# Kernel optimization log

Hardware: AMD Instinct MI355X
Metric: run time of the kernel (lower is better)

## Reference

```python
import jax, jax.numpy as jnp
import numpy as np
import math
from functools import partial

SIGMA0 = 12.0
KSIZE = int(2 * (4.0 * SIGMA0 + 0.5))  # 97, already odd
if KSIZE % 2 == 0:
    KSIZE -= 1


def _gauss1d(ksize, sigma):
    # kornia-style gaussian; ksize is odd so no half-pixel shift
    x = jnp.arange(ksize, dtype=jnp.float32) - ksize // 2
    g = jnp.exp(-(x ** 2) / (2.0 * sigma ** 2))
    return g / g.sum()


def _blur(x, sigma):
    # x: (N,1,H,W). filter2d with outer(kx,ky) kernel and constant(zero) border
    # == two separable 1D convs with zero 'SAME' padding.
    k = _gauss1d(KSIZE, sigma)
    dn = ('NCHW', 'OIHW', 'NCHW')
    x = jax.lax.conv_general_dilated(x, k[None, None, :, None], (1, 1), 'SAME', dimension_numbers=dn)
    x = jax.lax.conv_general_dilated(x, k[None, None, None, :], (1, 1), 'SAME', dimension_numbers=dn)
    return x


def _grid_sample_bilinear(img, grid):
    # img: (N,C,H,W); grid: (N,H,W,2) with last dim (x,y) in [-1,1], align_corners=True
    N, C, H, W = img.shape
    x = (grid[..., 0] + 1.0) * 0.5 * (W - 1)
    y = (grid[..., 1] + 1.0) * 0.5 * (H - 1)
    x0 = jnp.floor(x); y0 = jnp.floor(y)
    wx = x - x0; wy = y - y0
    x0i = jnp.clip(x0, 0, W - 1).astype(jnp.int32)
    x1i = jnp.clip(x0 + 1, 0, W - 1).astype(jnp.int32)
    y0i = jnp.clip(y0, 0, H - 1).astype(jnp.int32)
    y1i = jnp.clip(y0 + 1, 0, H - 1).astype(jnp.int32)
    flat = img.reshape(N, C, H * W)

    def gather(yi, xi):
        idx = (yi * W + xi).reshape(N, 1, H * W)
        return jnp.take_along_axis(flat, idx, axis=2).reshape(N, C, H, W)

    wx = wx[:, None]; wy = wy[:, None]  # broadcast over C
    top = gather(y0i, x0i) * (1 - wx) + gather(y0i, x1i) * wx
    bot = gather(y1i, x0i) * (1 - wx) + gather(y1i, x1i) * wx
    return top * (1 - wy) + bot * wy


def _elastic(t, d_rand, sigma, alpha):
    # t: (1,C,H,W); d_rand: (1,2,H,W) uniform [0,1]
    n, c, h, w = t.shape
    d = d_rand * 2.0 - 1.0
    dy = _blur(d[:, 0:1], sigma[0]) * alpha[0]   # (1,1,H,W)
    dx = _blur(d[:, 1:2], sigma[1]) * alpha[1]
    d_yx = jnp.concatenate([dy, dx], axis=1).transpose(0, 2, 3, 1)  # (1,H,W,2) = (dy,dx)
    xs = jnp.linspace(-1.0, 1.0, w, dtype=t.dtype)
    ys = jnp.linspace(-1.0, 1.0, h, dtype=t.dtype)
    gx, gy = jnp.meshgrid(xs, ys)  # (H,W)
    grid = jnp.stack([gx, gy], axis=-1)[None]  # (1,H,W,2) (x,y)
    # NOTE: faithful to source: dy is added to x-coord, dx to y-coord
    return _grid_sample_bilinear(t, jnp.clip(grid + d_yx, -1.0, 1.0))


def setup_inputs() -> dict:
    key = jax.random.key(0)
    k1, k2, k3 = jax.random.split(key, 3)
    H = W = 2048
    return {
        'image': jax.random.normal(k1, (3, H, W), dtype=jnp.float32),
        'mask': (jax.random.uniform(k2, (1, H, W)) > 0.5).astype(jnp.float32),
        'd_rand': jax.random.uniform(k3, (1, 2, H, W), dtype=jnp.float32),
        'log_sigma': jnp.full((2,), math.log(12.0), dtype=jnp.float32),
        'log_alpha': jnp.zeros((2,), dtype=jnp.float32),
    }


def reference(image, mask, d_rand, log_sigma, log_alpha):
    sigma = jnp.exp(log_sigma)
    alpha = jnp.exp(log_alpha)
    img_out = _elastic(image[None], d_rand, sigma, alpha)[0]
    msk_out = _elastic(mask[None], d_rand, sigma, alpha)[0]
    return (img_out, msk_out)
```

## Files before the change

### kernel.cpp

```cpp
#include <hip/hip_runtime.h>

#define H 2048
#define W 2048
#define KS 97
#define KH 48
#define KPAD 112
#define TR 16
#define NB_VB 1024
#define NB_PK 4096

__global__ __launch_bounds__(128) void make_weights_k(const float* __restrict__ log_sigma,
                                                      const float* __restrict__ log_alpha,
                                                      float* __restrict__ wts) {
    __shared__ float e0s[KS], e1s[KS];
    __shared__ float sums[2];
    const int t = threadIdx.x;
    const float s0 = expf(log_sigma[0]);
    const float s1 = expf(log_sigma[1]);
    if (t < KS) {
        const float xx = (float)(t - KH);
        e0s[t] = expf(-(xx * xx) / (2.f * s0 * s0));
        e1s[t] = expf(-(xx * xx) / (2.f * s1 * s1));
    }
    __syncthreads();
    if (t == 0) {
        float a = 0.f, b = 0.f;
        for (int k = 0; k < KS; ++k) { a += e0s[k]; b += e1s[k]; }
        sums[0] = a; sums[1] = b;
    }
    __syncthreads();
    if (t < KPAD) {
        wts[t]        = (t < KS) ? e0s[t] / sums[0] : 0.f;
        wts[KPAD + t] = (t < KS) ? e1s[t] / sums[1] : 0.f;
    }
    if (t == 0) {
        wts[2 * KPAD]     = expf(log_alpha[0]);
        wts[2 * KPAD + 1] = expf(log_alpha[1]);
    }
}

template <bool GUARD>
__device__ __forceinline__ float2 vload_row(const float* __restrict__ src, int row, int col) {
    float2 v = make_float2(0.f, 0.f);
    if (!GUARD || ((unsigned)row < (unsigned)H)) {
        const float2 r2 = *(const float2*)(src + (size_t)row * W + col);
        v.x = fmaf(r2.x, 2.f, -1.f);
        v.y = fmaf(r2.y, 2.f, -1.f);
    }
    return v;
}

template <bool GUARD>
__device__ __forceinline__ void vblur_body(const float* __restrict__ src,
                                           const float* __restrict__ g,
                                           float* __restrict__ dst,
                                           int col, int i0) {
    const int base = i0 - KH;
    float2 win[16];
    float2 acc[TR];
#pragma unroll
    for (int t = 0; t < TR; ++t) acc[t] = make_float2(0.f, 0.f);
#pragma unroll
    for (int t = 0; t < 15; ++t) win[t] = vload_row<GUARD>(src, base + t, col);

    for (int m = 0; m < KPAD / 16; ++m) {
        const int kb = m * 16;
#pragma unroll
        for (int r = 0; r < 16; ++r) {
            const int k = kb + r;
            win[(r + 15) & 15] = vload_row<GUARD>(src, base + k + 15, col);
            const float gk = g[k];
#pragma unroll
            for (int t = 0; t < TR; ++t) {
                const float2 u = win[(r + t) & 15];
                acc[t].x = fmaf(gk, u.x, acc[t].x);
                acc[t].y = fmaf(gk, u.y, acc[t].y);
            }
        }
    }
#pragma unroll
    for (int t = 0; t < TR; ++t)
        *(float2*)(dst + (size_t)(i0 + t) * W + col) = acc[t];
}

__global__ __launch_bounds__(256, 4) void pv_k(const float* __restrict__ drand,
                                               const float* __restrict__ wts,
                                               const float* __restrict__ image,
                                               const float* __restrict__ mask,
                                               float* __restrict__ tmp,
                                               float4* __restrict__ packed) {
    const size_t HW = (size_t)H * W;
    const int bid = blockIdx.x;
    if (bid < NB_VB) {
        const int c   = bid >> 9;
        const int id  = bid & 511;
        const int xcd = id & 7;
        const int seq = id >> 3;
        const int yb  = xcd * 16 + (seq >> 2);
        const int xb  = seq & 3;
        const int col = (xb * 256 + threadIdx.x) * 2;
        const int i0  = yb * TR;
        const float* __restrict__ src = drand + (size_t)c * HW;
        const float* __restrict__ g   = wts + c * KPAD;
        float* __restrict__ dst       = tmp + (size_t)c * HW;
        if (i0 >= KH && i0 + 78 <= H - 1)
            vblur_body<false>(src, g, dst, col, i0);
        else
            vblur_body<true>(src, g, dst, col, i0);
    } else {
        const size_t idx4 = ((size_t)(bid - NB_VB) * 256 + threadIdx.x) * 4;
        const float4 p0 = *(const float4*)(image + idx4);
        const float4 p1 = *(const float4*)(image + HW + idx4);
        const float4 p2 = *(const float4*)(image + 2 * HW + idx4);
        const float4 pm = *(const float4*)(mask + idx4);
        packed[idx4 + 0] = make_float4(p0.x, p1.x, p2.x, pm.x);
        packed[idx4 + 1] = make_float4(p0.y, p1.y, p2.y, pm.y);
        packed[idx4 + 2] = make_float4(p0.z, p1.z, p2.z, pm.z);
        packed[idx4 + 3] = make_float4(p0.w, p1.w, p2.w, pm.w);
    }
}

#define SW 2160
template <bool PACKED>
__global__ __launch_bounds__(512) void hblur_sample_k(const float* __restrict__ tmp,
                                                      const float* __restrict__ wts,
                                                      const float* __restrict__ image,
                                                      const float* __restrict__ mask,
                                                      const float4* __restrict__ packed,
                                                      float* __restrict__ out) {
    const int i   = (blockIdx.x & 7) * 256 + (blockIdx.x >> 3);
    const int tid = threadIdx.x;

    __shared__ __align__(16) float s0[SW];
    __shared__ __align__(16) float s1[SW];
    __shared__ __align__(16) float g0s[KPAD];
    __shared__ __align__(16) float g1s[KPAD];

    if (tid < KPAD) { g0s[tid] = wts[tid]; g1s[tid] = wts[KPAD + tid]; }

    const float* __restrict__ t0 = tmp + (size_t)i * W;
    const float* __restrict__ t1 = tmp + (size_t)H * W + (size_t)i * W;
    for (int idx = tid; idx < SW / 4; idx += 512) {
        const int colb = idx * 4 - KH;
        float4 v0 = make_float4(0.f, 0.f, 0.f, 0.f);
        float4 v1 = v0;
        if (colb >= 0 && colb + 3 < W) {
            v0 = *(const float4*)(t0 + colb);
            v1 = *(const float4*)(t1 + colb);
        }
        *(float4*)(s0 + idx * 4) = v0;
        *(float4*)(s1 + idx * 4) = v1;
    }
    __syncthreads();

    const int lb = tid * 4;

    float4 A0 = *(const float4*)(s0 + lb), B0 = *(const float4*)(s0 + lb + 4);
    float4 A1 = *(const float4*)(s1 + lb), B1 = *(const float4*)(s1 + lb + 4);
    float dy[4] = {0.f, 0.f, 0.f, 0.f}, dx[4] = {0.f, 0.f, 0.f, 0.f};

#pragma unroll
    for (int kg = 0; kg < 26; ++kg) {
        const int k0 = kg * 4;
        const float4 g0q = *(const float4*)(g0s + k0);
        const float4 g1q = *(const float4*)(g1s + k0);
        const float4 N0  = *(const float4*)(s0 + lb + k0 + 8);
        const float4 N1  = *(const float4*)(s1 + lb + k0 + 8);
        const float e0[8] = {A0.x, A0.y, A0.z, A0.w, B0.x, B0.y, B0.z, B0.w};
        const float e1[8] = {A1.x, A1.y, A1.z, A1.w, B1.x, B1.y, B1.z, B1.w};
#pragma unroll
        for (int j = 0; j < 4; ++j) {
            const float gj0 = j == 0 ? g0q.x : j == 1 ? g0q.y : j == 2 ? g0q.z : g0q.w;
            const float gj1 = j == 0 ? g1q.x : j == 1 ? g1q.y : j == 2 ? g1q.z : g1q.w;
#pragma unroll
            for (int c = 0; c < 4; ++c) {
                dy[c] = fmaf(gj0, e0[c + j], dy[c]);
                dx[c] = fmaf(gj1, e1[c + j], dx[c]);
            }
        }
        A0 = B0; B0 = N0; A1 = B1; B1 = N1;
    }

    const float a0 = wts[2 * KPAD];
    const float a1 = wts[2 * KPAD + 1];
    const float step = 2.f / 2047.f;
    float res[4][4];
#pragma unroll
    for (int c = 0; c < 4; ++c) {
        const int j = lb + c;
        const float dyc = dy[c] * a0;
        const float dxc = dx[c] * a1;
        float xn = -1.f + (float)j * step + dyc;
        float yn = -1.f + (float)i * step + dxc;
        xn = fminf(fmaxf(xn, -1.f), 1.f);
        yn = fminf(fmaxf(yn, -1.f), 1.f);

        const float x = (xn + 1.f) * 0.5f * (float)(W - 1);
        const float y = (yn + 1.f) * 0.5f * (float)(H - 1);
        const float x0f = floorf(x), y0f = floorf(y);
        const float wx = x - x0f, wy = y - y0f;

        int x0 = (int)x0f, y0 = (int)y0f;
        int x1 = x0 + 1, y1 = y0 + 1;
        x0 = min(max(x0, 0), W - 1); x1 = min(max(x1, 0), W - 1);
        y0 = min(max(y0, 0), H - 1); y1 = min(max(y1, 0), H - 1);

        const float w00 = (1.f - wx) * (1.f - wy);
        const float w10 = wx * (1.f - wy);
        const float w01 = (1.f - wx) * wy;
        const float w11 = wx * wy;

        const size_t i00 = (size_t)y0 * W + x0;
        const size_t i10 = (size_t)y0 * W + x1;
        const size_t i01 = (size_t)y1 * W + x0;
        const size_t i11 = (size_t)y1 * W + x1;

        if (PACKED) {
            const float4 v00 = packed[i00], v10 = packed[i10];
            const float4 v01 = packed[i01], v11 = packed[i11];
            res[0][c] = v00.x * w00 + v10.x * w10 + v01.x * w01 + v11.x * w11;
            res[1][c] = v00.y * w00 + v10.y * w10 + v01.y * w01 + v11.y * w11;
            res[2][c] = v00.z * w00 + v10.z * w10 + v01.z * w01 + v11.z * w11;
            res[3][c] = v00.w * w00 + v10.w * w10 + v01.w * w01 + v11.w * w11;
        } else {
#pragma unroll
            for (int p = 0; p < 3; ++p) {
                const float* __restrict__ pl = image + (size_t)p * H * W;
                res[p][c] = pl[i00] * w00 + pl[i10] * w10 + pl[i01] * w01 + pl[i11] * w11;
            }
            res[3][c] = mask[i00] * w00 + mask[i10] * w10 + mask[i01] * w01 + mask[i11] * w11;
        }
    }

    const size_t o = (size_t)i * W + lb;
#pragma unroll
    for (int p = 0; p < 4; ++p)
        *(float4*)(out + (size_t)p * H * W + o) =
            make_float4(res[p][0], res[p][1], res[p][2], res[p][3]);
}

extern "C" void kernel_launch(void* const* d_in, const int* in_sizes, int n_in,
                              void* d_out, int out_size, void* d_ws, size_t ws_size,
                              hipStream_t stream) {
    const float* image     = (const float*)d_in[0];
    const float* mask      = (const float*)d_in[1];
    const float* drand     = (const float*)d_in[2];
    const float* log_sigma = (const float*)d_in[3];
    const float* log_alpha = (const float*)d_in[4];
    float* out = (float*)d_out;

    const size_t HW = (size_t)H * W;
    const bool can_pack = ws_size >= (6 * HW + 256) * sizeof(float);

    float4* packed; float* tmp; float* wts;
    if (can_pack) {
        packed = (float4*)d_ws;
        tmp    = (float*)d_ws + 4 * HW;
        wts    = tmp + 2 * HW;
    } else {
        packed = nullptr;
        tmp    = (float*)d_ws;
        wts    = tmp + 2 * HW;
    }

    make_weights_k<<<1, 128, 0, stream>>>(log_sigma, log_alpha, wts);
    pv_k<<<can_pack ? (NB_VB + NB_PK) : NB_VB, 256, 0, stream>>>(drand, wts, image, mask,
                                                                 tmp, packed);
    if (can_pack)
        hblur_sample_k<true><<<H, 512, 0, stream>>>(tmp, wts, image, mask, packed, out);
    else
        hblur_sample_k<false><<<H, 512, 0, stream>>>(tmp, wts, image, mask, packed, out);
}
```

Measured before the change: 246.1 us.

## Fold weight computation into blur kernels, widen hblur per-thread work, interleave pack blocks

Removes the separate make_weights kernel launch: each vertical-blur block and each hblur block now recomputes and normalizes the Gaussian taps in shared memory, and the alpha values, from log_sigma/log_alpha. The hblur/sample kernel moves to 256 threads with 8 outputs per thread and trims the tap loop to 104 taps, which gives more register reuse of the sliding window. Output stores become nontemporal. In pv_k, vertical-blur blocks are interleaved with pack blocks (one in five) and the occupancy hint is raised. The cost is redundant expf work per block and extra barriers, plus higher register pressure from the wider tile.

Result: slower. 376.0 us (+52.8%).

```diff
diff --git a/kernel.cpp b/kernel.cpp
--- a/kernel.cpp
+++ b/kernel.cpp
@@ -5,39 +5,12 @@
 #define KS 97
 #define KH 48
 #define KPAD 112
+#define KP2 104
 #define TR 16
 #define NB_VB 1024
 #define NB_PK 4096
 
-__global__ __launch_bounds__(128) void make_weights_k(const float* __restrict__ log_sigma,
-                                                      const float* __restrict__ log_alpha,
-                                                      float* __restrict__ wts) {
-    __shared__ float e0s[KS], e1s[KS];
-    __shared__ float sums[2];
-    const int t = threadIdx.x;
-    const float s0 = expf(log_sigma[0]);
-    const float s1 = expf(log_sigma[1]);
-    if (t < KS) {
-        const float xx = (float)(t - KH);
-        e0s[t] = expf(-(xx * xx) / (2.f * s0 * s0));
-        e1s[t] = expf(-(xx * xx) / (2.f * s1 * s1));
-    }
-    __syncthreads();
-    if (t == 0) {
-        float a = 0.f, b = 0.f;
-        for (int k = 0; k < KS; ++k) { a += e0s[k]; b += e1s[k]; }
-        sums[0] = a; sums[1] = b;
-    }
-    __syncthreads();
-    if (t < KPAD) {
-        wts[t]        = (t < KS) ? e0s[t] / sums[0] : 0.f;
-        wts[KPAD + t] = (t < KS) ? e1s[t] / sums[1] : 0.f;
-    }
-    if (t == 0) {
-        wts[2 * KPAD]     = expf(log_alpha[0]);
-        wts[2 * KPAD + 1] = expf(log_alpha[1]);
-    }
-}
+typedef float nfloat4 __attribute__((ext_vector_type(4)));
 
 template <bool GUARD>
 __device__ __forceinline__ float2 vload_row(const float* __restrict__ src, int row, int col) {
@@ -83,32 +56,55 @@
         *(float2*)(dst + (size_t)(i0 + t) * W + col) = acc[t];
 }
 
-__global__ __launch_bounds__(256, 4) void pv_k(const float* __restrict__ drand,
-                                               const float* __restrict__ wts,
+template <bool PACK>
+__global__ __launch_bounds__(256, 6) void pv_k(const float* __restrict__ drand,
+                                               const float* __restrict__ log_sigma,
                                                const float* __restrict__ image,
                                                const float* __restrict__ mask,
                                                float* __restrict__ tmp,
                                                float4* __restrict__ packed) {
     const size_t HW = (size_t)H * W;
     const int bid = blockIdx.x;
-    if (bid < NB_VB) {
-        const int c   = bid >> 9;
-        const int id  = bid & 511;
+    const bool is_vb = !PACK || (bid % 5 == 0);
+    if (is_vb) {
+        const int vb  = PACK ? (bid / 5) : bid;
+        const int c   = vb >> 9;
+        const int id  = vb & 511;
         const int xcd = id & 7;
         const int seq = id >> 3;
         const int yb  = xcd * 16 + (seq >> 2);
         const int xb  = seq & 3;
         const int col = (xb * 256 + threadIdx.x) * 2;
         const int i0  = yb * TR;
+        const int t   = threadIdx.x;
+
+        __shared__ float gs[KPAD];
+        __shared__ float sinv;
+        const float sig = expf(log_sigma[c]);
+        if (t < KPAD) {
+            const float xx = (float)(t - KH);
+            gs[t] = (t < KS) ? expf(-(xx * xx) / (2.f * sig * sig)) : 0.f;
+        }
+        __syncthreads();
+        if (t < 64) {
+            float v = gs[t] + ((t + 64 < KPAD) ? gs[t + 64] : 0.f);
+#pragma unroll
+            for (int off = 32; off; off >>= 1) v += __shfl_down(v, off);
+            if (t == 0) sinv = 1.f / v;
+        }
+        __syncthreads();
+        if (t < KPAD) gs[t] *= sinv;
+        __syncthreads();
+
         const float* __restrict__ src = drand + (size_t)c * HW;
-        const float* __restrict__ g   = wts + c * KPAD;
         float* __restrict__ dst       = tmp + (size_t)c * HW;
         if (i0 >= KH && i0 + 78 <= H - 1)
-            vblur_body<false>(src, g, dst, col, i0);
+            vblur_body<false>(src, gs, dst, col, i0);
         else
-            vblur_body<true>(src, g, dst, col, i0);
+            vblur_body<true>(src, gs, dst, col, i0);
     } else {
-        const size_t idx4 = ((size_t)(bid - NB_VB) * 256 + threadIdx.x) * 4;
+        const int pk = bid - (bid / 5) - 1;
+        const size_t idx4 = ((size_t)pk * 256 + threadIdx.x) * 4;
         const float4 p0 = *(const float4*)(image + idx4);
         const float4 p1 = *(const float4*)(image + HW + idx4);
         const float4 p2 = *(const float4*)(image + 2 * HW + idx4);
@@ -122,8 +118,9 @@
 
 #define SW 2160
 template <bool PACKED>
-__global__ __launch_bounds__(512) void hblur_sample_k(const float* __restrict__ tmp,
-                                                      const float* __restrict__ wts,
+__global__ __launch_bounds__(256) void hblur_sample_k(const float* __restrict__ tmp,
+                                                      const float* __restrict__ log_sigma,
+                                                      const float* __restrict__ log_alpha,
                                                       const float* __restrict__ image,
                                                       const float* __restrict__ mask,
                                                       const float4* __restrict__ packed,
@@ -133,14 +130,41 @@
 
     __shared__ __align__(16) float s0[SW];
     __shared__ __align__(16) float s1[SW];
-    __shared__ __align__(16) float g0s[KPAD];
-    __shared__ __align__(16) float g1s[KPAD];
-
-    if (tid < KPAD) { g0s[tid] = wts[tid]; g1s[tid] = wts[KPAD + tid]; }
+    __shared__ __align__(16) float g0s[KP2];
+    __shared__ __align__(16) float g1s[KP2];
+    __shared__ float inv0, inv1, a0s, a1s;
+
+    {
+        const float sg0 = expf(log_sigma[0]);
+        const float sg1 = expf(log_sigma[1]);
+        if (tid < KP2) {
+            const float xx = (float)(tid - KH);
+            const bool in = tid < KS;
+            g0s[tid] = in ? expf(-(xx * xx) / (2.f * sg0 * sg0)) : 0.f;
+            g1s[tid] = in ? expf(-(xx * xx) / (2.f * sg1 * sg1)) : 0.f;
+        }
+        if (tid == 128) a0s = expf(log_alpha[0]);
+        if (tid == 129) a1s = expf(log_alpha[1]);
+        __syncthreads();
+        if (tid < 64) {
+            float v = g0s[tid] + ((tid + 64 < KP2) ? g0s[tid + 64] : 0.f);
+#pragma unroll
+            for (int off = 32; off; off >>= 1) v += __shfl_down(v, off);
+            if (tid == 0) inv0 = 1.f / v;
+        } else if (tid < 128) {
+            const int l = tid - 64;
+            float v = g1s[l] + ((l + 64 < KP2) ? g1s[l + 64] : 0.f);
+#pragma unroll
+            for (int off = 32; off; off >>= 1) v += __shfl_down(v, off);
+            if (l == 0) inv1 = 1.f / v;
+        }
+        __syncthreads();
+        if (tid < KP2) { g0s[tid] *= inv0; g1s[tid] *= inv1; }
+    }
 
     const float* __restrict__ t0 = tmp + (size_t)i * W;
     const float* __restrict__ t1 = tmp + (size_t)H * W + (size_t)i * W;
-    for (int idx = tid; idx < SW / 4; idx += 512) {
+    for (int idx = tid; idx < SW / 4; idx += 256) {
         const int colb = idx * 4 - KH;
         float4 v0 = make_float4(0.f, 0.f, 0.f, 0.f);
         float4 v1 = v0;
@@ -153,90 +177,102 @@
     }
     __syncthreads();
 
-    const int lb = tid * 4;
-
-    float4 A0 = *(const float4*)(s0 + lb), B0 = *(const float4*)(s0 + lb + 4);
-    float4 A1 = *(const float4*)(s1 + lb), B1 = *(const float4*)(s1 + lb + 4);
-    float dy[4] = {0.f, 0.f, 0.f, 0.f}, dx[4] = {0.f, 0.f, 0.f, 0.f};
-
-#pragma unroll
-    for (int kg = 0; kg < 26; ++kg) {
+    const int lb = tid * 8;
+
+    float4 A0 = *(const float4*)(s0 + lb), B0 = *(const float4*)(s0 + lb + 4),
+           C0 = *(const float4*)(s0 + lb + 8);
+    float4 A1 = *(const float4*)(s1 + lb), B1 = *(const float4*)(s1 + lb + 4),
+           C1 = *(const float4*)(s1 + lb + 8);
+    float dy[8], dx[8];
+#pragma unroll
+    for (int c = 0; c < 8; ++c) { dy[c] = 0.f; dx[c] = 0.f; }
+
+#pragma unroll
+    for (int kg = 0; kg < KP2 / 4; ++kg) {
         const int k0 = kg * 4;
         const float4 g0q = *(const float4*)(g0s + k0);
         const float4 g1q = *(const float4*)(g1s + k0);
-        const float4 N0  = *(const float4*)(s0 + lb + k0 + 8);
-        const float4 N1  = *(const float4*)(s1 + lb + k0 + 8);
-        const float e0[8] = {A0.x, A0.y, A0.z, A0.w, B0.x, B0.y, B0.z, B0.w};
-        const float e1[8] = {A1.x, A1.y, A1.z, A1.w, B1.x, B1.y, B1.z, B1.w};
+        const float4 N0  = *(const float4*)(s0 + lb + k0 + 12);
+        const float4 N1  = *(const float4*)(s1 + lb + k0 + 12);
+        const float e0[12] = {A0.x, A0.y, A0.z, A0.w, B0.x, B0.y, B0.z, B0.w,
+                              C0.x, C0.y, C0.z, C0.w};
+        const float e1[12] = {A1.x, A1.y, A1.z, A1.w, B1.x, B1.y, B1.z, B1.w,
+                              C1.x, C1.y, C1.z, C1.w};
 #pragma unroll
         for (int j = 0; j < 4; ++j) {
             const float gj0 = j == 0 ? g0q.x : j == 1 ? g0q.y : j == 2 ? g0q.z : g0q.w;
             const float gj1 = j == 0 ? g1q.x : j == 1 ? g1q.y : j == 2 ? g1q.z : g1q.w;
 #pragma unroll
-            for (int c = 0; c < 4; ++c) {
+            for (int c = 0; c < 8; ++c) {
                 dy[c] = fmaf(gj0, e0[c + j], dy[c]);
                 dx[c] = fmaf(gj1, e1[c + j], dx[c]);
             }
         }
-        A0 = B0; B0 = N0; A1 = B1; B1 = N1;
-    }
-
-    const float a0 = wts[2 * KPAD];
-    const float a1 = wts[2 * KPAD + 1];
+        A0 = B0; B0 = C0; C0 = N0;
+        A1 = B1; B1 = C1; C1 = N1;
+    }
+
+    const float a0 = a0s;
+    const float a1 = a1s;
     const float step = 2.f / 2047.f;
-    float res[4][4];
-#pragma unroll
-    for (int c = 0; c < 4; ++c) {
-        const int j = lb + c;
-        const float dyc = dy[c] * a0;
-        const float dxc = dx[c] * a1;
-        float xn = -1.f + (float)j * step + dyc;
-        float yn = -1.f + (float)i * step + dxc;
-        xn = fminf(fmaxf(xn, -1.f), 1.f);
-        yn = fminf(fmaxf(yn, -1.f), 1.f);
-
-        const float x = (xn + 1.f) * 0.5f * (float)(W - 1);
-        const float y = (yn + 1.f) * 0.5f * (float)(H - 1);
-        const float x0f = floorf(x), y0f = floorf(y);
-        const float wx = x - x0f, wy = y - y0f;
-
-        int x0 = (int)x0f, y0 = (int)y0f;
-        int x1 = x0 + 1, y1 = y0 + 1;
-        x0 = min(max(x0, 0), W - 1); x1 = min(max(x1, 0), W - 1);
-        y0 = min(max(y0, 0), H - 1); y1 = min(max(y1, 0), H - 1);
-
-        const float w00 = (1.f - wx) * (1.f - wy);
-        const float w10 = wx * (1.f - wy);
-        const float w01 = (1.f - wx) * wy;
-        const float w11 = wx * wy;
-
-        const size_t i00 = (size_t)y0 * W + x0;
-        const size_t i10 = (size_t)y0 * W + x1;
-        const size_t i01 = (size_t)y1 * W + x0;
-        const size_t i11 = (size_t)y1 * W + x1;
-
-        if (PACKED) {
-            const float4 v00 = packed[i00], v10 = packed[i10];
-            const float4 v01 = packed[i01], v11 = packed[i11];
-            res[0][c] = v00.x * w00 + v10.x * w10 + v01.x * w01 + v11.x * w11;
-            res[1][c] = v00.y * w00 + v10.y * w10 + v01.y * w01 + v11.y * w11;
-            res[2][c] = v00.z * w00 + v10.z * w10 + v01.z * w01 + v11.z * w11;
-            res[3][c] = v00.w * w00 + v10.w * w10 + v01.w * w01 + v11.w * w11;
-        } else {
-#pragma unroll
-            for (int p = 0; p < 3; ++p) {
-                const float* __restrict__ pl = image + (size_t)p * H * W;
-                res[p][c] = pl[i00] * w00 + pl[i10] * w10 + pl[i01] * w01 + pl[i11] * w11;
+#pragma unroll
+    for (int grp = 0; grp < 2; ++grp) {
+        float res[4][4];
+#pragma unroll
+        for (int cc = 0; cc < 4; ++cc) {
+            const int c = grp * 4 + cc;
+            const int j = lb + c;
+            const float dyc = dy[c] * a0;
+            const float dxc = dx[c] * a1;
+            float xn = -1.f + (float)j * step + dyc;
+            float yn = -1.f + (float)i * step + dxc;
+            xn = fminf(fmaxf(xn, -1.f), 1.f);
+            yn = fminf(fmaxf(yn, -1.f), 1.f);
+
+            const float x = (xn + 1.f) * 0.5f * (float)(W - 1);
+            const float y = (yn + 1.f) * 0.5f * (float)(H - 1);
+            const float x0f = floorf(x), y0f = floorf(y);
+            const float wx = x - x0f, wy = y - y0f;
+
+            int x0 = (int)x0f, y0 = (int)y0f;
+            int x1 = x0 + 1, y1 = y0 + 1;
+            x0 = min(max(x0, 0), W - 1); x1 = min(max(x1, 0), W - 1);
+            y0 = min(max(y0, 0), H - 1); y1 = min(max(y1, 0), H - 1);
+
+            const float w00 = (1.f - wx) * (1.f - wy);
+            const float w10 = wx * (1.f - wy);
+            const float w01 = (1.f - wx) * wy;
+            const float w11 = wx * wy;
+
+            const size_t i00 = (size_t)y0 * W + x0;
+            const size_t i10 = (size_t)y0 * W + x1;
+            const size_t i01 = (size_t)y1 * W + x0;
+            const size_t i11 = (size_t)y1 * W + x1;
+
+            if (PACKED) {
+                const float4 v00 = packed[i00], v10 = packed[i10];
+                const float4 v01 = packed[i01], v11 = packed[i11];
+                res[0][cc] = v00.x * w00 + v10.x * w10 + v01.x * w01 + v11.x * w11;
+                res[1][cc] = v00.y * w00 + v10.y * w10 + v01.y * w01 + v11.y * w11;
+                res[2][cc] = v00.z * w00 + v10.z * w10 + v01.z * w01 + v11.z * w11;
+                res[3][cc] = v00.w * w00 + v10.w * w10 + v01.w * w01 + v11.w * w11;
+            } else {
+#pragma unroll
+                for (int p = 0; p < 3; ++p) {
+                    const float* __restrict__ pl = image + (size_t)p * H * W;
+                    res[p][cc] = pl[i00] * w00 + pl[i10] * w10 + pl[i01] * w01 + pl[i11] * w11;
+                }
+                res[3][cc] = mask[i00] * w00 + mask[i10] * w10 + mask[i01] * w01 + mask[i11] * w11;
             }
-            res[3][c] = mask[i00] * w00 + mask[i10] * w10 + mask[i01] * w01 + mask[i11] * w11;
-        }
-    }
-
-    const size_t o = (size_t)i * W + lb;
-#pragma unroll
-    for (int p = 0; p < 4; ++p)
-        *(float4*)(out + (size_t)p * H * W + o) =
-            make_float4(res[p][0], res[p][1], res[p][2], res[p][3]);
+        }
+        const size_t o = (size_t)i * W + lb + grp * 4;
+#pragma unroll
+        for (int p = 0; p < 4; ++p) {
+            nfloat4 v;
+            v.x = res[p][0]; v.y = res[p][1]; v.z = res[p][2]; v.w = res[p][3];
+            __builtin_nontemporal_store(v, (nfloat4*)(out + (size_t)p * H * W + o));
+        }
+    }
 }
 
 extern "C" void kernel_launch(void* const* d_in, const int* in_sizes, int n_in,
@@ -250,24 +286,26 @@
     float* out = (float*)d_out;
 
     const size_t HW = (size_t)H * W;
-    const bool can_pack = ws_size >= (6 * HW + 256) * sizeof(float);
-
-    float4* packed; float* tmp; float* wts;
+    const bool can_pack = ws_size >= 6 * HW * sizeof(float);
+
+    float4* packed; float* tmp;
     if (can_pack) {
         packed = (float4*)d_ws;
         tmp    = (float*)d_ws + 4 * HW;
-        wts    = tmp + 2 * HW;
     } else {
         packed = nullptr;
         tmp    = (float*)d_ws;
-        wts    = tmp + 2 * HW;
-    }
-
-    make_weights_k<<<1, 128, 0, stream>>>(log_sigma, log_alpha, wts);
-    pv_k<<<can_pack ? (NB_VB + NB_PK) : NB_VB, 256, 0, stream>>>(drand, wts, image, mask,
-                                                                 tmp, packed);
-    if (can_pack)
-        hblur_sample_k<true><<<H, 512, 0, stream>>>(tmp, wts, image, mask, packed, out);
-    else
-        hblur_sample_k<false><<<H, 512, 0, stream>>>(tmp, wts, image, mask, packed, out);
-}
+    }
+
+    if (can_pack) {
+        pv_k<true><<<NB_VB + NB_PK, 256, 0, stream>>>(drand, log_sigma, image, mask,
+                                                      tmp, packed);
+        hblur_sample_k<true><<<H, 256, 0, stream>>>(tmp, log_sigma, log_alpha,
+                                                    image, mask, packed, out);
+    } else {
+        pv_k<false><<<NB_VB, 256, 0, stream>>>(drand, log_sigma, image, mask,
+                                               tmp, packed);
+        hblur_sample_k<false><<<H, 256, 0, stream>>>(tmp, log_sigma, log_alpha,
+                                                     image, mask, packed, out);
+    }
+}
```
